# Kernel optimization log

Hardware: AMD Instinct MI355X
Metric: run time of the kernel (lower is better)

Reference implementation:

```python
import jax, jax.numpy as jnp
import numpy as np

NUM_HEADS = 8
BLOCK = 16


def setup_inputs() -> dict:
    key = jax.random.key(0)
    kx, k1, k2, k3 = jax.random.split(key, 4)
    B, S, D = 8, 8192, 512
    x = jax.random.normal(kx, (B, S, D), dtype=jnp.float32)
    # nn.MultiheadAttention parameters (xavier-ish scale)
    w_in = jax.random.normal(k1, (3 * D, D), dtype=jnp.float32) / np.sqrt(D)
    b_in = jnp.zeros((3 * D,), dtype=jnp.float32)
    w_out = jax.random.normal(k2, (D, D), dtype=jnp.float32) / np.sqrt(D)
    b_out = jnp.zeros((D,), dtype=jnp.float32)
    return {"x": x, "w_in": w_in, "b_in": b_in, "w_out": w_out, "b_out": b_out}


def reference(x, w_in, b_in, w_out, b_out):
    B, S, D = x.shape
    H = NUM_HEADS
    hd = D // H
    nb = S // BLOCK
    # [B, nb, L, D] — independent attention within each length-BLOCK chunk
    xb = x.reshape(B, nb, BLOCK, D)
    qkv = jnp.einsum('bnld,ed->bnle', xb, w_in) + b_in  # e = 3D
    q, k, v = jnp.split(qkv, 3, axis=-1)
    q = q.reshape(B, nb, BLOCK, H, hd)
    k = k.reshape(B, nb, BLOCK, H, hd)
    v = v.reshape(B, nb, BLOCK, H, hd)
    scale = 1.0 / np.sqrt(hd).astype(np.float32)
    scores = jnp.einsum('bnqhd,bnkhd->bnhqk', q * scale, k)
    attn = jax.nn.softmax(scores, axis=-1)
    ctx = jnp.einsum('bnhqk,bnkhd->bnqhd', attn, v).reshape(B, nb, BLOCK, D)
    out = jnp.einsum('bnld,od->bnlo', ctx, w_out) + b_out
    return out.reshape(B, S, D)
```

## Files before the change

### kernel.cpp

```cpp
#include <hip/hip_runtime.h>
#include <hip/hip_bf16.h>

typedef __attribute__((ext_vector_type(4))) float f32x4;
typedef __attribute__((ext_vector_type(8))) short short8;
typedef __attribute__((ext_vector_type(4))) short short4v;
using bf16 = __hip_bfloat16;

__device__ __forceinline__ short f2bf(float x) {
  union { bf16 h; short s; } u;
  u.h = __float2bfloat16(x);
  return u.s;
}

__device__ __forceinline__ void gload16(const void* g, void* l) {
  __builtin_amdgcn_global_load_lds(
      (const __attribute__((address_space(1))) void*)g,
      (__attribute__((address_space(3))) void*)l, 16, 0, 0);
}

__global__ void cvt_f32_to_bf16(const float* __restrict__ src,
                                bf16* __restrict__ dst, int n4) {
  int i = blockIdx.x * blockDim.x + threadIdx.x;
  const int stride = gridDim.x * blockDim.x;
  for (; i < n4; i += stride) {
    f32x4 v = ((const f32x4*)src)[i];
    short4v o;
    o[0] = f2bf(v[0]); o[1] = f2bf(v[1]); o[2] = f2bf(v[2]); o[3] = f2bf(v[3]);
    ((short4v*)dst)[i] = o;
  }
}

template<bool OUT_BF16>
__global__ __launch_bounds__(256) void gemm_bt(
    const bf16* __restrict__ A, int lda,
    const bf16* __restrict__ B, int ldb,
    const float* __restrict__ bias,
    void* __restrict__ Cv, int ldc, int K, int nbx)
{
  __shared__ __align__(16) bf16 lA[128 * 64];
  __shared__ __align__(16) bf16 lB[128 * 64];
  const int tid  = threadIdx.x;
  const int wave = tid >> 6;
  const int lane = tid & 63;

  const int nwg = gridDim.x;
  const int d   = blockIdx.x;
  const int w   = (d & 7) * (nwg >> 3) + (d >> 3);
  const int bm  = (w / nbx) * 128;
  const int bn  = (w % nbx) * 128;

  const int wm = (wave >> 1) * 64;
  const int wn = (wave & 1) * 64;
  const int l15 = lane & 15;
  const int kg  = lane >> 4;
  const int rx  = l15 & 7;

  f32x4 acc[4][4];
#pragma unroll
  for (int i = 0; i < 4; ++i)
#pragma unroll
    for (int j = 0; j < 4; ++j)
      acc[i][j] = (f32x4)0.f;

  const int srow = lane >> 3;
  const int scol = ((lane & 7) ^ (srow & 7)) * 8;

  for (int kt = 0; kt < K; kt += 64) {
    __syncthreads();
#pragma unroll
    for (int it = 0; it < 4; ++it) {
      const int seg = it * 4 + wave;
      const int row = seg * 8 + srow;
      gload16(A + (size_t)(bm + row) * lda + kt + scol, &lA[seg * 512]);
      gload16(B + (size_t)(bn + row) * ldb + kt + scol, &lB[seg * 512]);
    }
    __syncthreads();
#pragma unroll
    for (int ks = 0; ks < 2; ++ks) {
      short8 af[4], bfr[4];
      const int slot = ks * 4 + kg;
      const int po   = (slot ^ rx) * 8;
#pragma unroll
      for (int mi = 0; mi < 4; ++mi)
        af[mi] = *(const short8*)&lA[(wm + mi * 16 + l15) * 64 + po];
#pragma unroll
      for (int ni = 0; ni < 4; ++ni)
        bfr[ni] = *(const short8*)&lB[(wn + ni * 16 + l15) * 64 + po];
#pragma unroll
      for (int mi = 0; mi < 4; ++mi)
#pragma unroll
        for (int ni = 0; ni < 4; ++ni)
          acc[mi][ni] = __builtin_amdgcn_mfma_f32_16x16x32_bf16(
              bfr[ni], af[mi], acc[mi][ni], 0, 0, 0);
    }
  }

#pragma unroll
  for (int mi = 0; mi < 4; ++mi) {
    const size_t mrow = (size_t)bm + wm + mi * 16 + l15;
#pragma unroll
    for (int ni = 0; ni < 4; ++ni) {
      const int nb = bn + wn + ni * 16 + kg * 4;
      f32x4 bv = *(const f32x4*)&bias[nb];
      f32x4 r = acc[mi][ni] + bv;
      if constexpr (OUT_BF16) {
        short4v o;
        o[0] = f2bf(r[0]); o[1] = f2bf(r[1]); o[2] = f2bf(r[2]); o[3] = f2bf(r[3]);
        *(short4v*)((bf16*)Cv + mrow * ldc + nb) = o;
      } else {
        *(f32x4*)((float*)Cv + mrow * ldc + nb) = r;
      }
    }
  }
}

__global__ __launch_bounds__(256) void attn_kernel(bf16* __restrict__ qkv)
{
  const int tid  = threadIdx.x;
  const int wave = tid >> 6;
  const int lane = tid & 63;
  const int l15  = lane & 15;
  const int kg   = lane >> 4;
  const size_t mbase = (size_t)blockIdx.x * 16;

  f32x4 ctxv[2][4];

#pragma unroll
  for (int hi = 0; hi < 2; ++hi) {
    const int h = wave + hi * 4;
    const bf16* qp = qkv + (mbase + l15) * 1536 + h * 64 + kg * 8;
    short8 qf0 = *(const short8*)qp;
    short8 qf1 = *(const short8*)(qp + 32);
    short8 kf0 = *(const short8*)(qp + 512);
    short8 kf1 = *(const short8*)(qp + 544);

    f32x4 st = (f32x4)0.f;
    st = __builtin_amdgcn_mfma_f32_16x16x32_bf16(kf0, qf0, st, 0, 0, 0);
    st = __builtin_amdgcn_mfma_f32_16x16x32_bf16(kf1, qf1, st, 0, 0, 0);

    float s[4];
#pragma unroll
    for (int r = 0; r < 4; ++r) s[r] = st[r] * 0.125f;
    float mx = fmaxf(fmaxf(s[0], s[1]), fmaxf(s[2], s[3]));
    mx = fmaxf(mx, __shfl_xor(mx, 16));
    mx = fmaxf(mx, __shfl_xor(mx, 32));
    float p[4], sum = 0.f;
#pragma unroll
    for (int r = 0; r < 4; ++r) { p[r] = __expf(s[r] - mx); sum += p[r]; }
    sum += __shfl_xor(sum, 16);
    sum += __shfl_xor(sum, 32);
    const float inv = 1.f / sum;

    short4v pf;
#pragma unroll
    for (int r = 0; r < 4; ++r) pf[r] = f2bf(p[r] * inv);

    const bf16* vp = qkv + mbase * 1536 + 1024 + h * 64;
#pragma unroll
    for (int dt = 0; dt < 4; ++dt) {
      short4v vf;
#pragma unroll
      for (int jj = 0; jj < 4; ++jj)
        vf[jj] = *(const short*)(vp + (size_t)(kg * 4 + jj) * 1536 + dt * 16 + l15);
      f32x4 c = (f32x4)0.f;
      c = __builtin_amdgcn_mfma_f32_16x16x16bf16_1k(pf, vf, c, 0, 0, 0);
      ctxv[hi][dt] = c;
    }
  }

  __syncthreads();

#pragma unroll
  for (int hi = 0; hi < 2; ++hi) {
    const int h = wave + hi * 4;
#pragma unroll
    for (int dt = 0; dt < 4; ++dt) {
#pragma unroll
      for (int r = 0; r < 4; ++r) {
        ((short*)qkv)[(mbase + kg * 4 + r) * 1536 + h * 64 + dt * 16 + l15] =
            f2bf(ctxv[hi][dt][r]);
      }
    }
  }
}

extern "C" void kernel_launch(void* const* d_in, const int* in_sizes, int n_in,
                              void* d_out, int out_size, void* d_ws, size_t ws_size,
                              hipStream_t stream) {
  (void)in_sizes; (void)n_in; (void)out_size; (void)ws_size;
  const float* x     = (const float*)d_in[0];
  const float* w_in  = (const float*)d_in[1];
  const float* b_in  = (const float*)d_in[2];
  const float* w_out = (const float*)d_in[3];
  const float* b_out = (const float*)d_in[4];
  float* out = (float*)d_out;

  char* ws = (char*)d_ws;
  bf16* qkv   = (bf16*)ws;
  bf16* winb  = (bf16*)(ws + (size_t)65536 * 1536 * 2);
  bf16* woutb = (bf16*)(ws + (size_t)65536 * 1536 * 2 + (size_t)786432 * 2);
  bf16* xb = (bf16*)d_out;

  cvt_f32_to_bf16<<<768, 256, 0, stream>>>(w_in, winb, 786432 / 4);
  cvt_f32_to_bf16<<<256, 256, 0, stream>>>(w_out, woutb, 262144 / 4);
  cvt_f32_to_bf16<<<4096, 256, 0, stream>>>(x, xb, (65536 * 512) / 4);

  gemm_bt<true><<<6144, 256, 0, stream>>>(
      xb, 512, winb, 512, b_in, (void*)qkv, 1536, 512, 12);

  attn_kernel<<<4096, 256, 0, stream>>>(qkv);

  gemm_bt<false><<<2048, 256, 0, stream>>>(
      qkv, 1536, woutb, 512, b_out, (void*)out, 512, 512, 4);
}
```

Measured before the change: 314.3 us.

## Rewrite GEMM as 256x256 tile, 512-thread kernel with 4-stage LDS pipeline

New measurement: 288.3 us. -8.3%, faster.

```diff
diff --git a/kernel.cpp b/kernel.cpp
--- a/kernel.cpp
+++ b/kernel.cpp
@@ -31,76 +31,112 @@
 }
 
 template<bool OUT_BF16>
-__global__ __launch_bounds__(256) void gemm_bt(
+__global__ __launch_bounds__(512) void gemm_bt(
     const bf16* __restrict__ A, int lda,
     const bf16* __restrict__ B, int ldb,
     const float* __restrict__ bias,
-    void* __restrict__ Cv, int ldc, int K, int nbx)
+    void* __restrict__ Cv, int ldc, int nbx)
 {
-  __shared__ __align__(16) bf16 lA[128 * 64];
-  __shared__ __align__(16) bf16 lB[128 * 64];
+  __shared__ __align__(16) bf16 lA[4][256 * 32];
+  __shared__ __align__(16) bf16 lB[4][256 * 32];
+
   const int tid  = threadIdx.x;
-  const int wave = tid >> 6;
   const int lane = tid & 63;
+  const int w    = tid >> 6;
+  const int wr   = w >> 2;
+  const int wc   = w & 3;
+  const int l15  = lane & 15;
+  const int kg   = lane >> 4;
+  const int po   = (kg ^ ((l15 >> 1) & 3)) * 8;
 
   const int nwg = gridDim.x;
-  const int d   = blockIdx.x;
-  const int w   = (d & 7) * (nwg >> 3) + (d >> 3);
-  const int bm  = (w / nbx) * 128;
-  const int bn  = (w % nbx) * 128;
-
-  const int wm = (wave >> 1) * 64;
-  const int wn = (wave & 1) * 64;
-  const int l15 = lane & 15;
-  const int kg  = lane >> 4;
-  const int rx  = l15 & 7;
-
-  f32x4 acc[4][4];
-#pragma unroll
-  for (int i = 0; i < 4; ++i)
-#pragma unroll
-    for (int j = 0; j < 4; ++j)
-      acc[i][j] = (f32x4)0.f;
-
-  const int srow = lane >> 3;
-  const int scol = ((lane & 7) ^ (srow & 7)) * 8;
-
-  for (int kt = 0; kt < K; kt += 64) {
-    __syncthreads();
-#pragma unroll
-    for (int it = 0; it < 4; ++it) {
-      const int seg = it * 4 + wave;
-      const int row = seg * 8 + srow;
-      gload16(A + (size_t)(bm + row) * lda + kt + scol, &lA[seg * 512]);
-      gload16(B + (size_t)(bn + row) * ldb + kt + scol, &lB[seg * 512]);
-    }
-    __syncthreads();
-#pragma unroll
-    for (int ks = 0; ks < 2; ++ks) {
-      short8 af[4], bfr[4];
-      const int slot = ks * 4 + kg;
-      const int po   = (slot ^ rx) * 8;
-#pragma unroll
-      for (int mi = 0; mi < 4; ++mi)
-        af[mi] = *(const short8*)&lA[(wm + mi * 16 + l15) * 64 + po];
+  const int dd  = blockIdx.x;
+  const int wid = (dd & 7) * (nwg >> 3) + (dd >> 3);
+  const size_t bm = (size_t)(wid / nbx) * 256;
+  const size_t bn = (size_t)(wid % nbx) * 256;
+
+  const int srow = w * 16 + (lane >> 2);
+  const int scol = ((lane & 3) ^ ((lane >> 3) & 3)) * 8;
+  const int wofs = w * 512;
+
+  const bf16* Ab = A + (bm + srow) * lda + scol;
+  const bf16* Bb = B + (bn + srow) * ldb + scol;
+
+  f32x4 acc[8][4];
+#pragma unroll
+  for (int i = 0; i < 8; ++i)
+#pragma unroll
+    for (int j = 0; j < 4; ++j) acc[i][j] = (f32x4)0.f;
+
+  short8 af[8], bq[4];
+
+#define SA(buf, h, kt) gload16(Ab + (size_t)((h) * 128) * lda + (kt), \
+                               &lA[buf][(h) * 4096 + wofs])
+#define SB(buf, h, kt) gload16(Bb + (size_t)((h) * 128) * ldb + (kt), \
+                               &lB[buf][(h) * 4096 + wofs])
+
+#define CLOSE_V(N) do { \
+    __builtin_amdgcn_sched_barrier(0); \
+    asm volatile("s_waitcnt vmcnt(" #N ")" ::: "memory"); \
+    __builtin_amdgcn_sched_barrier(0); \
+    __builtin_amdgcn_s_barrier(); \
+    __builtin_amdgcn_sched_barrier(0); \
+    asm volatile("" ::: "memory"); } while (0)
+
+  SA(0, 0, 0);  SA(0, 1, 0);  SB(0, 0, 0);  SB(0, 1, 0);
+  SA(1, 0, 32); SA(1, 1, 32); SB(1, 0, 32); SB(1, 1, 32);
+  SA(2, 0, 64); SA(2, 1, 64); SB(2, 0, 64); SB(2, 1, 64);
+  CLOSE_V(8);
+
+#pragma unroll
+  for (int t = 0; t < 16; ++t) {
+    const int cur = t & 3, pf = (t + 3) & 3;
+    const int kt3 = (t + 3) * 32;
+
+#pragma unroll
+    for (int mi = 0; mi < 8; ++mi)
+      af[mi] = *(const short8*)&lA[cur][(wr * 128 + mi * 16 + l15) * 32 + po];
+#pragma unroll
+    for (int ni = 0; ni < 4; ++ni)
+      bq[ni] = *(const short8*)&lB[cur][(wc * 64 + ni * 16 + l15) * 32 + po];
+
+    if (t < 13) { SA(pf, 0, kt3); SB(pf, 0, kt3); }
+
+    __builtin_amdgcn_s_setprio(1);
+#pragma unroll
+    for (int mi = 0; mi < 4; ++mi)
 #pragma unroll
       for (int ni = 0; ni < 4; ++ni)
-        bfr[ni] = *(const short8*)&lB[(wn + ni * 16 + l15) * 64 + po];
-#pragma unroll
-      for (int mi = 0; mi < 4; ++mi)
-#pragma unroll
-        for (int ni = 0; ni < 4; ++ni)
-          acc[mi][ni] = __builtin_amdgcn_mfma_f32_16x16x32_bf16(
-              bfr[ni], af[mi], acc[mi][ni], 0, 0, 0);
-    }
-  }
-
-#pragma unroll
-  for (int mi = 0; mi < 4; ++mi) {
-    const size_t mrow = (size_t)bm + wm + mi * 16 + l15;
+        acc[mi][ni] = __builtin_amdgcn_mfma_f32_16x16x32_bf16(
+            bq[ni], af[mi], acc[mi][ni], 0, 0, 0);
+    __builtin_amdgcn_s_setprio(0);
+
+    if (t < 13) { SA(pf, 1, kt3); SB(pf, 1, kt3); }
+
+    __builtin_amdgcn_s_setprio(1);
+#pragma unroll
+    for (int mi = 4; mi < 8; ++mi)
+#pragma unroll
+      for (int ni = 0; ni < 4; ++ni)
+        acc[mi][ni] = __builtin_amdgcn_mfma_f32_16x16x32_bf16(
+            bq[ni], af[mi], acc[mi][ni], 0, 0, 0);
+    __builtin_amdgcn_s_setprio(0);
+
+    if (t <= 12)      CLOSE_V(8);
+    else if (t == 13) CLOSE_V(4);
+    else if (t == 14) CLOSE_V(0);
+  }
+
+#undef SA
+#undef SB
+#undef CLOSE_V
+
+#pragma unroll
+  for (int mi = 0; mi < 8; ++mi) {
+    const size_t mrow = bm + wr * 128 + mi * 16 + l15;
 #pragma unroll
     for (int ni = 0; ni < 4; ++ni) {
-      const int nb = bn + wn + ni * 16 + kg * 4;
+      const int nb = (int)bn + wc * 64 + ni * 16 + kg * 4;
       f32x4 bv = *(const f32x4*)&bias[nb];
       f32x4 r = acc[mi][ni] + bv;
       if constexpr (OUT_BF16) {
@@ -205,11 +241,11 @@
   cvt_f32_to_bf16<<<256, 256, 0, stream>>>(w_out, woutb, 262144 / 4);
   cvt_f32_to_bf16<<<4096, 256, 0, stream>>>(x, xb, (65536 * 512) / 4);
 
-  gemm_bt<true><<<6144, 256, 0, stream>>>(
-      xb, 512, winb, 512, b_in, (void*)qkv, 1536, 512, 12);
+  gemm_bt<true><<<1536, 512, 0, stream>>>(
+      xb, 512, winb, 512, b_in, (void*)qkv, 1536, 6);
 
   attn_kernel<<<4096, 256, 0, stream>>>(qkv);
 
-  gemm_bt<false><<<2048, 256, 0, stream>>>(
-      qkv, 1536, woutb, 512, b_out, (void*)out, 512, 512, 4);
-}
+  gemm_bt<false><<<512, 512, 0, stream>>>(
+      qkv, 1536, woutb, 512, b_out, (void*)out, 512, 2);
+}
```
